# Optimization experiments

Hardware: AMD Instinct MI355X
Metric: run time of the kernel (lower is better)

Reference implementation:

```python
import jax, jax.numpy as jnp
import numpy as np

EPS = 0.1
MAX_ITER = 100
THRESH = 0.1


def setup_inputs() -> dict:
    key = jax.random.key(0)
    k1, k2 = jax.random.split(key)
    N = 4096
    x = jax.random.normal(k1, (N, N), dtype=jnp.float32)
    y = jax.random.normal(k2, (N, N), dtype=jnp.float32)
    return {"x": x, "y": y}


def _sinkhorn(x, y):
    # forward softmaxes inputs along last dim
    x = jax.nn.softmax(x, axis=-1)
    y = jax.nn.softmax(y, axis=-1)
    # squared-euclidean cost |x_i - y_j|^2, expanded to avoid an [N,N,D] broadcast
    x2 = jnp.sum(x * x, axis=-1)  # [n]
    y2 = jnp.sum(y * y, axis=-1)  # [m]
    C = x2[:, None] + y2[None, :] - 2.0 * (x @ y.T)  # [n, m]
    n = x.shape[-1]  # source sizes mu/nu by the FEATURE dim (requires n == m == d)
    log_mu = jnp.log(jnp.full((n,), 1.0 / n, dtype=C.dtype) + 1e-8)
    log_nu = log_mu

    def M(u, v):
        # faithful to source: both u and v broadcast over the COLUMN axis
        return (-C + u[None, :] + v[None, :]) / EPS

    def step(carry, _):
        u, v, done = carry
        u1 = u
        u_new = EPS * (log_mu - jax.nn.logsumexp(M(u, v), axis=-1)) + u
        v_new = EPS * (log_nu - jax.nn.logsumexp(M(u_new, v).T, axis=-1)) + v
        # torch: (u-u1).abs().sum(-1).mean() with implicit batch of 1 == plain sum
        err = jnp.sum(jnp.abs(u_new - u1))
        u = jnp.where(done, u, u_new)
        v = jnp.where(done, v, v_new)
        return (u, v, done | (err < THRESH)), None

    init = (jnp.zeros((n,), C.dtype), jnp.zeros((n,), C.dtype), jnp.array(False))
    (u, v, _), _ = jax.lax.scan(step, init, None, length=MAX_ITER)
    pi = jnp.exp(M(u, v))  # [n, m] (torch returns [1, n, m]; batch dim squeezed)
    cost = jnp.sum(pi * C)  # cost.mean() over the singleton batch == scalar sum
    return cost, pi, C


def reference(x, y):
    return _sinkhorn(x, y)
```

## Files before the change

### kernel.cpp

```cpp
#include <hip/hip_runtime.h>
#include <math.h>

#define NN 4096

typedef __bf16 bf16;
typedef __attribute__((ext_vector_type(4))) __bf16 bf16x4;
typedef __attribute__((ext_vector_type(8))) __bf16 bf16x8;
typedef __attribute__((ext_vector_type(4))) float f32x4;

__device__ __forceinline__ void gld16(const void* g, void* l) {
  __builtin_amdgcn_global_load_lds((const __attribute__((address_space(1))) void*)g,
                                   (__attribute__((address_space(3))) void*)l, 16, 0, 0);
}


__device__ __forceinline__ double blockSumD(double v) {
  __shared__ double w[4];
  #pragma unroll
  for (int o = 32; o > 0; o >>= 1) v += __shfl_down(v, o, 64);
  __syncthreads();
  if ((threadIdx.x & 63) == 0) w[threadIdx.x >> 6] = v;
  __syncthreads();
  return w[0] + w[1] + w[2] + w[3];
}

__device__ __forceinline__ float blockMaxF(float v) {
  __shared__ float w[4];
  #pragma unroll
  for (int o = 32; o > 0; o >>= 1) v = fmaxf(v, __shfl_down(v, o, 64));
  __syncthreads();
  if ((threadIdx.x & 63) == 0) w[threadIdx.x >> 6] = v;
  __syncthreads();
  return fmaxf(fmaxf(w[0], w[1]), fmaxf(w[2], w[3]));
}


__global__ void softmax_rows(const float* __restrict__ x, const float* __restrict__ y,
                             bf16* __restrict__ xh, bf16* __restrict__ yh,
                             float* __restrict__ rowsq) {
  int row = blockIdx.x;
  int r = (row < NN) ? row : row - NN;
  const f32x4* __restrict__ src = (const f32x4*)(((row < NN) ? x : y) + (size_t)r * NN);
  bf16x4* __restrict__ dst = (bf16x4*)(((row < NN) ? xh : yh) + (size_t)r * NN);
  int t = threadIdx.x;

  f32x4 v[4];
  float m = -3.402823466e38f;
  #pragma unroll
  for (int j = 0; j < 4; ++j) {
    v[j] = src[t + 256 * j];
    m = fmaxf(fmaxf(fmaxf(m, v[j].x), fmaxf(v[j].y, v[j].z)), v[j].w);
  }
  float M = blockMaxF(m);

  float s = 0.0f;
  #pragma unroll
  for (int j = 0; j < 4; ++j) {
    v[j].x = expf(v[j].x - M); v[j].y = expf(v[j].y - M);
    v[j].z = expf(v[j].z - M); v[j].w = expf(v[j].w - M);
    s += (v[j].x + v[j].y) + (v[j].z + v[j].w);
  }
  double S = blockSumD((double)s);
  float inv = (float)(1.0 / S);

  float q = 0.0f;
  #pragma unroll
  for (int j = 0; j < 4; ++j) {
    f32x4 p = v[j] * inv;
    bf16x4 h;
    h.x = (bf16)p.x; h.y = (bf16)p.y; h.z = (bf16)p.z; h.w = (bf16)p.w;
    dst[t + 256 * j] = h;
    q += (p.x * p.x + p.y * p.y) + (p.z * p.z + p.w * p.w);
  }
  double Q = blockSumD((double)q);
  if (t == 0) rowsq[row] = (float)Q;
}


__global__ __launch_bounds__(256) void gemm_bt(const bf16* __restrict__ A,
                                               const bf16* __restrict__ B,
                                               const float* __restrict__ rowsq,
                                               float* __restrict__ C,
                                               float* __restrict__ colpart) {
  __shared__ __align__(16) bf16 As[128 * 64];
  __shared__ __align__(16) bf16 Bs[128 * 64];
  __shared__ float lsc[2][128];
  int t = threadIdx.x;
  int i0 = blockIdx.y * 128;
  int j0 = blockIdx.x * 128;
  int w = t >> 6, l = t & 63;
  int mrow = (w >> 1) * 64, ncol = (w & 1) * 64;
  int lr = l & 15, lq = l >> 4;

  f32x4 acc[4][4] = {};

  for (int kc = 0; kc < NN; kc += 64) {
    __syncthreads();
    #pragma unroll
    for (int q = 0; q < 4; ++q) {
      int c = t + 256 * q;
      int row = c >> 3;
      int jg = (c & 7) ^ (row & 7);
      gld16(A + (size_t)(i0 + row) * NN + kc + jg * 8, (char*)As + c * 16);
    }
    #pragma unroll
    for (int q = 0; q < 4; ++q) {
      int c = t + 256 * q;
      int row = c >> 3;
      int jg = (c & 7) ^ (row & 7);
      gld16(B + (size_t)(j0 + row) * NN + kc + jg * 8, (char*)Bs + c * 16);
    }
    __syncthreads();

    #pragma unroll
    for (int s = 0; s < 2; ++s) {
      bf16x8 af[4], bg[4];
      #pragma unroll
      for (int i = 0; i < 4; ++i) {
        int ra = mrow + 16 * i + lr;
        int ja = (s * 4 + lq) ^ (ra & 7);
        af[i] = *(const bf16x8*)((const char*)As + (ra * 8 + ja) * 16);
        int rb = ncol + 16 * i + lr;
        int jb = (s * 4 + lq) ^ (rb & 7);
        bg[i] = *(const bf16x8*)((const char*)Bs + (rb * 8 + jb) * 16);
      }
      #pragma unroll
      for (int i = 0; i < 4; ++i)
        #pragma unroll
        for (int jj = 0; jj < 4; ++jj)
          acc[i][jj] = __builtin_amdgcn_mfma_f32_16x16x32_bf16(af[i], bg[jj], acc[i][jj], 0, 0, 0);
    }
  }

  float y2v[4], ec[4] = {0.f, 0.f, 0.f, 0.f};
  #pragma unroll
  for (int jj = 0; jj < 4; ++jj) y2v[jj] = rowsq[NN + j0 + ncol + 16 * jj + lr];
  #pragma unroll
  for (int i = 0; i < 4; ++i) {
    #pragma unroll
    for (int r = 0; r < 4; ++r) {
      int grow = i0 + mrow + 16 * i + lq * 4 + r;
      float x2 = rowsq[grow];
      size_t rowoff = (size_t)grow * NN + j0 + ncol;
      #pragma unroll
      for (int jj = 0; jj < 4; ++jj) {
        float cv = x2 + y2v[jj] - 2.0f * acc[i][jj][r];
        C[rowoff + 16 * jj + lr] = cv;
        ec[jj] += expf(-10.0f * cv);
      }
    }
  }
  #pragma unroll
  for (int jj = 0; jj < 4; ++jj) {
    ec[jj] += __shfl_xor(ec[jj], 16, 64);
    ec[jj] += __shfl_xor(ec[jj], 32, 64);
  }
  if (lq == 0) {
    #pragma unroll
    for (int jj = 0; jj < 4; ++jj) lsc[w >> 1][ncol + 16 * jj + lr] = ec[jj];
  }
  __syncthreads();
  if (t < 128) colpart[(size_t)blockIdx.y * NN + j0 + t] = lsc[0][t] + lsc[1][t];
}


__global__ void col_lse_final(const float* __restrict__ colpart, float* __restrict__ sdf) {
  int col = blockIdx.x * 256 + threadIdx.x;
  double s = 0.0;
  #pragma unroll
  for (int ch = 0; ch < 32; ++ch) s += (double)colpart[(size_t)ch * NN + col];
  double log_nu = log(1.0 / (double)NN + 1e-8);
  sdf[col] = (float)(log_nu - log(s));
}


__global__ void pi_cost(const float* __restrict__ Cm, const float* __restrict__ sdf,
                        float* __restrict__ pi, double* __restrict__ costpart) {
  size_t idx0 = (size_t)blockIdx.x * 2048 + threadIdx.x;
  float facc = 0.0f;
  #pragma unroll
  for (int j = 0; j < 8; ++j) {
    size_t idx = idx0 + 256 * j;
    float c = Cm[idx];
    int col = (int)(idx & (NN - 1));
    float p = expf(fmaf(-10.0f, c, sdf[col]));
    pi[idx] = p;
    facc = fmaf(p, c, facc);
  }
  double total = blockSumD((double)facc);
  if (threadIdx.x == 0) costpart[blockIdx.x] = total;
}


__global__ void cost_final(const double* __restrict__ costpart, float* __restrict__ out) {
  double s = 0.0;
  #pragma unroll
  for (int j = 0; j < 32; ++j) s += costpart[threadIdx.x + 256 * j];
  double total = blockSumD(s);
  if (threadIdx.x == 0) out[0] = (float)total;
}


extern "C" void kernel_launch(void* const* d_in, const int* in_sizes, int n_in,
                              void* d_out, int out_size, void* d_ws, size_t ws_size,
                              hipStream_t stream) {
  const float* x = (const float*)d_in[0];
  const float* y = (const float*)d_in[1];
  float* out = (float*)d_out;
  float* pi = out + 1;
  float* Cm = out + 1 + (size_t)NN * NN;

  char* ws = (char*)d_ws;
  bf16* xh = (bf16*)ws;
  bf16* yh = xh + (size_t)NN * NN;
  size_t off = (size_t)NN * NN * 2 * 2;
  float* rowsq = (float*)(ws + off);       off += 2 * NN * 4;
  float* sdf = (float*)(ws + off);         off += NN * 4;
  float* colpart = (float*)(ws + off);     off += 32 * NN * 4;
  double* costpart = (double*)(ws + off);  off += 8192 * 8;

  hipLaunchKernelGGL(softmax_rows, dim3(2 * NN), dim3(256), 0, stream, x, y, xh, yh, rowsq);
  hipLaunchKernelGGL(gemm_bt, dim3(32, 32), dim3(256), 0, stream, xh, yh, rowsq, Cm, colpart);
  hipLaunchKernelGGL(col_lse_final, dim3(16), dim3(256), 0, stream, colpart, sdf);
  hipLaunchKernelGGL(pi_cost, dim3(8192), dim3(256), 0, stream, Cm, sdf, pi, costpart);
  hipLaunchKernelGGL(cost_final, dim3(1), dim3(256), 0, stream, costpart, out);
}
```

Baseline: 398.7 us.

## Fuse column LSE and cost reduction into pi kernel, use fast exp

Folds the column log-sum-exp finalisation and the final cost reduction into the pi/cost kernel. Each 128x128 tile block now recomputes its own column offsets from the partials and atomically adds its cost into the output, which is zeroed in the softmax kernel. That removes two small launches and the intermediate buffers. It also switches expf to __expf in the softmax, GEMM epilogue and pi kernels. The trade-offs are a float atomic sum that is not deterministic and redundant column-partial reads across row tiles. Each block also handles a larger tile, so the grid is smaller.

```diff
diff --git a/kernel.cpp b/kernel.cpp
--- a/kernel.cpp
+++ b/kernel.cpp
@@ -37,12 +37,13 @@
 
 __global__ void softmax_rows(const float* __restrict__ x, const float* __restrict__ y,
                              bf16* __restrict__ xh, bf16* __restrict__ yh,
-                             float* __restrict__ rowsq) {
+                             float* __restrict__ rowsq, float* __restrict__ out) {
   int row = blockIdx.x;
+  int t = threadIdx.x;
+  if (row == 0 && t == 0) out[0] = 0.0f;
   int r = (row < NN) ? row : row - NN;
   const f32x4* __restrict__ src = (const f32x4*)(((row < NN) ? x : y) + (size_t)r * NN);
   bf16x4* __restrict__ dst = (bf16x4*)(((row < NN) ? xh : yh) + (size_t)r * NN);
-  int t = threadIdx.x;
 
   f32x4 v[4];
   float m = -3.402823466e38f;
@@ -56,8 +57,8 @@
   float s = 0.0f;
   #pragma unroll
   for (int j = 0; j < 4; ++j) {
-    v[j].x = expf(v[j].x - M); v[j].y = expf(v[j].y - M);
-    v[j].z = expf(v[j].z - M); v[j].w = expf(v[j].w - M);
+    v[j].x = __expf(v[j].x - M); v[j].y = __expf(v[j].y - M);
+    v[j].z = __expf(v[j].z - M); v[j].w = __expf(v[j].w - M);
     s += (v[j].x + v[j].y) + (v[j].z + v[j].w);
   }
   double S = blockSumD((double)s);
@@ -146,7 +147,7 @@
       for (int jj = 0; jj < 4; ++jj) {
         float cv = x2 + y2v[jj] - 2.0f * acc[i][jj][r];
         C[rowoff + 16 * jj + lr] = cv;
-        ec[jj] += expf(-10.0f * cv);
+        ec[jj] += __expf(-10.0f * cv);
       }
     }
   }
@@ -164,40 +165,34 @@
 }
 
 
-__global__ void col_lse_final(const float* __restrict__ colpart, float* __restrict__ sdf) {
-  int col = blockIdx.x * 256 + threadIdx.x;
-  double s = 0.0;
-  #pragma unroll
-  for (int ch = 0; ch < 32; ++ch) s += (double)colpart[(size_t)ch * NN + col];
-  double log_nu = log(1.0 / (double)NN + 1e-8);
-  sdf[col] = (float)(log_nu - log(s));
-}
-
-
-__global__ void pi_cost(const float* __restrict__ Cm, const float* __restrict__ sdf,
-                        float* __restrict__ pi, double* __restrict__ costpart) {
-  size_t idx0 = (size_t)blockIdx.x * 2048 + threadIdx.x;
+__global__ void pi_cost_fused(const float* __restrict__ Cm, const float* __restrict__ colpart,
+                              float* __restrict__ pi, float* __restrict__ out) {
+  __shared__ float sdl[128];
+  int t = threadIdx.x;
+  int j0 = blockIdx.x * 128;
+  int r0 = blockIdx.y * 128;
+  if (t < 128) {
+    double s = 0.0;
+    #pragma unroll
+    for (int ch = 0; ch < 32; ++ch) s += (double)colpart[(size_t)ch * NN + j0 + t];
+    sdl[t] = (float)(-8.317725207557924 - log(s));
+  }
+  __syncthreads();
+
+  int col = t & 127, rh = t >> 7;
+  float sj = sdl[col];
   float facc = 0.0f;
-  #pragma unroll
-  for (int j = 0; j < 8; ++j) {
-    size_t idx = idx0 + 256 * j;
+  #pragma unroll 8
+  for (int rr = 0; rr < 64; ++rr) {
+    int row = r0 + rr * 2 + rh;
+    size_t idx = (size_t)row * NN + j0 + col;
     float c = Cm[idx];
-    int col = (int)(idx & (NN - 1));
-    float p = expf(fmaf(-10.0f, c, sdf[col]));
+    float p = __expf(fmaf(-10.0f, c, sj));
     pi[idx] = p;
     facc = fmaf(p, c, facc);
   }
   double total = blockSumD((double)facc);
-  if (threadIdx.x == 0) costpart[blockIdx.x] = total;
-}
-
-
-__global__ void cost_final(const double* __restrict__ costpart, float* __restrict__ out) {
-  double s = 0.0;
-  #pragma unroll
-  for (int j = 0; j < 32; ++j) s += costpart[threadIdx.x + 256 * j];
-  double total = blockSumD(s);
-  if (threadIdx.x == 0) out[0] = (float)total;
+  if (t == 0) atomicAdd(out, (float)total);
 }
 
 
@@ -215,13 +210,9 @@
   bf16* yh = xh + (size_t)NN * NN;
   size_t off = (size_t)NN * NN * 2 * 2;
   float* rowsq = (float*)(ws + off);       off += 2 * NN * 4;
-  float* sdf = (float*)(ws + off);         off += NN * 4;
   float* colpart = (float*)(ws + off);     off += 32 * NN * 4;
-  double* costpart = (double*)(ws + off);  off += 8192 * 8;
-
-  hipLaunchKernelGGL(softmax_rows, dim3(2 * NN), dim3(256), 0, stream, x, y, xh, yh, rowsq);
+
+  hipLaunchKernelGGL(softmax_rows, dim3(2 * NN), dim3(256), 0, stream, x, y, xh, yh, rowsq, out);
   hipLaunchKernelGGL(gemm_bt, dim3(32, 32), dim3(256), 0, stream, xh, yh, rowsq, Cm, colpart);
-  hipLaunchKernelGGL(col_lse_final, dim3(16), dim3(256), 0, stream, colpart, sdf);
-  hipLaunchKernelGGL(pi_cost, dim3(8192), dim3(256), 0, stream, Cm, sdf, pi, costpart);
-  hipLaunchKernelGGL(cost_final, dim3(1), dim3(256), 0, stream, costpart, out);
-}
+  hipLaunchKernelGGL(pi_cost_fused, dim3(32, 32), dim3(256), 0, stream, Cm, colpart, pi, out);
+}
```

Measured after the change: 403.6 us. Within noise of the previous version (+1.2%).
